# Kernel optimization log

Measured on AMD Instinct MI355X. Metric: run time of the kernel, lower is better.

## Reference

```python
import jax, jax.numpy as jnp
import numpy as np

B, C, H, W = 4, 384, 64, 64
NH = 8
HD = C // NH
SR = 2
SCALE = HD ** -0.5
Hs, Ws = H // SR, W // SR
NK = Hs * Ws


def setup_inputs() -> dict:
    key = jax.random.key(0)
    ks = jax.random.split(key, 8)
    s = 0.02
    return {
        "x": jax.random.normal(ks[0], (B, C, H, W), jnp.float32),
        "Wq": jax.random.normal(ks[1], (C, C), jnp.float32) * s,
        "Wk": jax.random.normal(ks[2], (C, C), jnp.float32) * s,
        "Wv": jax.random.normal(ks[3], (C, C), jnp.float32) * s,
        "Wsr": jax.random.normal(ks[4], (C, C, SR, SR), jnp.float32) * s,
        "bsr": jnp.zeros((C,), jnp.float32),
        "Wp": jax.random.normal(ks[5], (C, C), jnp.float32) * s,
        "bp": jnp.zeros((C,), jnp.float32),
        "rel_h": jax.random.normal(ks[6], (1, NH, HD, 1, Hs), jnp.float32),
        "rel_w": jax.random.normal(ks[7], (1, NH, HD, Ws, 1), jnp.float32),
    }


def _mhsa(x, Wq, Wk, Wv, Wsr, bsr, Wp, bp, rel_h, rel_w):
    Bq = x.shape[0]
    # 1x1 conv == channel matmul
    q = jnp.einsum('oc,bchw->bohw', Wq, x).reshape(Bq, NH, HD, H * W)
    # spatial reduction: Conv2d(kernel=SR, stride=SR); norm defaults to Identity
    xsr = jax.lax.conv_general_dilated(
        x, Wsr, window_strides=(SR, SR), padding='VALID',
        dimension_numbers=('NCHW', 'OIHW', 'NCHW')) + bsr[None, :, None, None]
    k = jnp.einsum('oc,bchw->bohw', Wk, xsr).reshape(Bq, NH, HD, NK)
    v = jnp.einsum('oc,bchw->bohw', Wv, xsr).reshape(Bq, NH, HD, NK)
    # relative positional bias fused into keys
    pos = (rel_h + rel_w).reshape(1, NH, HD, NK)
    k = (k + pos) * SCALE
    # attn[b,h,n,m] = q^T k, softmax over keys (dropout is identity at p=0)
    attn = jax.nn.softmax(jnp.einsum('bhdn,bhdm->bhnm', q, k), axis=-1)
    out = jnp.einsum('bhdm,bhnm->bhdn', v, attn).reshape(Bq, C, H, W)
    out = jnp.einsum('oc,bchw->bohw', Wp, out) + bp[None, :, None, None]
    return out


def reference(x, Wq, Wk, Wv, Wsr, bsr, Wp, bp, rel_h, rel_w):
    return _mhsa(x, Wq, Wk, Wv, Wsr, bsr, Wp, bp, rel_h, rel_w)
```

## Files before the change

### kernel.cpp

```cpp
#include <hip/hip_runtime.h>
#include <hip/hip_bf16.h>
#include <math.h>

typedef __attribute__((ext_vector_type(8))) short b16x8;
typedef __attribute__((ext_vector_type(4))) short b16x4;
typedef __attribute__((ext_vector_type(4))) float floatx4;
typedef __attribute__((ext_vector_type(16))) float f32x16;

constexpr int BATCH = 4, CCH = 384, NQ = 4096, NHD = 8, HDIM = 48, NK = 1024;
constexpr float SCALE_L2E = 0.14433756729740643f * 1.4426950408889634f;

__device__ inline unsigned short f2bf(float f) {
    unsigned u = __builtin_bit_cast(unsigned, f);
    u += 0x7fffu + ((u >> 16) & 1u);
    return (unsigned short)(u >> 16);
}

__device__ __forceinline__ void g2lds16(const void* g, void* l) {
    __builtin_amdgcn_global_load_lds(
        (const __attribute__((address_space(1))) unsigned int*)g,
        (__attribute__((address_space(3))) unsigned int*)l, 16, 0, 0);
}

__global__ void prep_kern(const float* __restrict__ Wq, const float* __restrict__ Wk,
                          const float* __restrict__ Wv, const float* __restrict__ Wsr,
                          const float* __restrict__ Wp, const float* __restrict__ x,
                          short* __restrict__ WqB, short* __restrict__ WkvB,
                          short* __restrict__ WsrB, short* __restrict__ WpB,
                          short* __restrict__ xT) {
    int job = blockIdx.y;
    if (job == 5) {
        for (int i = blockIdx.x * 256 + threadIdx.x; i < BATCH * 4096 * 48;
             i += 576 * 256) {
            int b = i / (4096 * 48);
            int rem = i - b * (4096 * 48);
            int c8 = rem / 4096, s = rem - c8 * 4096;
            b16x8 pk;
            #pragma unroll
            for (int e = 0; e < 8; e++)
                pk[e] = (short)f2bf(x[((size_t)b * CCH + c8 * 8 + e) * NQ + s]);
            *(b16x8*)(xT + ((size_t)b * NQ + s) * CCH + c8 * 8) = pk;
        }
        return;
    }
    if (job == 3) {
        for (int i = blockIdx.x * 256 + threadIdx.x; i < 589824; i += gridDim.x * 256) {
            int o = i / 1536, r = i - o * 1536;
            WsrB[o * 1536 + (r & 3) * 384 + (r >> 2)] = (short)f2bf(Wsr[i]);
        }
        return;
    }
    const float* src; short* dst;
    if (job == 0)      { src = Wq;  dst = WqB; }
    else if (job == 1) { src = Wk;  dst = WkvB; }
    else if (job == 2) { src = Wv;  dst = WkvB + 147456; }
    else               { src = Wp;  dst = WpB; }
    for (int i = blockIdx.x * 256 + threadIdx.x; i < 147456; i += gridDim.x * 256)
        dst[i] = (short)f2bf(src[i]);
}

__global__ __launch_bounds__(256, 2) void fused_gemm1(
    const short* __restrict__ WsrB, const short* __restrict__ WqB,
    const short* __restrict__ xT, const float* __restrict__ bsr,
    short* __restrict__ xsrT, short* __restrict__ qTb)
{
    __shared__ short At[128 * 64];
    __shared__ short Bt[128 * 64];
    const int b = blockIdx.z;
    const int id = blockIdx.x;
    const bool conv = id < 24;
    const int sx = conv ? (id & 7) : ((id - 24) & 31);
    const int oy = conv ? (id >> 3) : ((id - 24) >> 5);
    const int Ks = conv ? 1536 : 384;
    const int S  = conv ? NK : NQ;
    const short* A = conv ? WsrB : WqB;
    short* Yt = conv ? xsrT : qTb;
    const int o0 = oy * 128, s0 = sx * 128;
    const int t = threadIdx.x, wave = t >> 6, lane = t & 63, g = lane >> 4, li = lane & 15;
    const int wr = wave >> 1, wc = wave & 1;
    floatx4 acc[4][4] = {};
    const short* Bbase = xT + (size_t)b * NQ * CCH;

    for (int k0 = 0; k0 < Ks; k0 += 64) {
        __syncthreads();
        #pragma unroll
        for (int it = 0; it < 4; it++) {
            int task = it * 256 + t;
            int row = task >> 3, ch = task & 7;
            int cont = ch ^ (row & 7);
            g2lds16(A + (size_t)(o0 + row) * Ks + k0 + cont * 8, At + task * 8);
        }
        #pragma unroll
        for (int it = 0; it < 4; it++) {
            int task = it * 256 + t;
            int row = task >> 3, ch = task & 7;
            int cont = ch ^ (row & 7);
            if (conv) {
                int ssr = s0 + row;
                int hs = ssr >> 5, wsv = ssr & 31;
                int k = k0 + cont * 8;
                int p = k / 384, coff = k - p * 384;
                g2lds16(Bbase + (size_t)((2 * hs + (p >> 1)) * 64 + 2 * wsv + (p & 1)) * 384 + coff,
                        Bt + task * 8);
            } else {
                g2lds16(Bbase + (size_t)(s0 + row) * 384 + k0 + cont * 8, Bt + task * 8);
            }
        }
        __syncthreads();
        #pragma unroll
        for (int kk = 0; kk < 2; kk++) {
            b16x8 af[4], bf[4];
            #pragma unroll
            for (int mi = 0; mi < 4; mi++) {
                int r = wr * 64 + mi * 16 + li;
                af[mi] = *(const b16x8*)(At + r * 64 + (((kk * 4 + g) ^ (r & 7)) * 8));
            }
            #pragma unroll
            for (int nf = 0; nf < 4; nf++) {
                int r = wc * 64 + nf * 16 + li;
                bf[nf] = *(const b16x8*)(Bt + r * 64 + (((kk * 4 + g) ^ (r & 7)) * 8));
            }
            #pragma unroll
            for (int mi = 0; mi < 4; mi++)
                #pragma unroll
                for (int nf = 0; nf < 4; nf++)
                    acc[mi][nf] = __builtin_amdgcn_mfma_f32_16x16x32_bf16(af[mi], bf[nf], acc[mi][nf], 0, 0, 0);
        }
    }

    #pragma unroll
    for (int mi = 0; mi < 4; mi++) {
        #pragma unroll
        for (int nf = 0; nf < 4; nf++) {
            int o = o0 + wr * 64 + mi * 16 + g * 4;
            int s = s0 + wc * 64 + nf * 16 + li;
            b16x4 pk;
            #pragma unroll
            for (int j = 0; j < 4; j++) {
                float v = acc[mi][nf][j];
                if (conv) v += bsr[o + j];
                pk[j] = (short)f2bf(v);
            }
            *(b16x4*)(Yt + ((size_t)b * S + s) * CCH + o) = pk;
        }
    }
}

__global__ __launch_bounds__(256, 2) void kv_gemm(
    const short* __restrict__ WkvB, const short* __restrict__ xsrT,
    const float* __restrict__ relh, const float* __restrict__ relw,
    short* __restrict__ kTb, short* __restrict__ vCb)
{
    __shared__ short At[128 * 64];
    __shared__ short Bt[128 * 64];
    const int b = blockIdx.z, o0 = blockIdx.y * 128, s0 = blockIdx.x * 128;
    const int t = threadIdx.x, wave = t >> 6, lane = t & 63, g = lane >> 4, li = lane & 15;
    const int wr = wave >> 1, wc = wave & 1;
    floatx4 acc[4][4] = {};
    const short* Bbase = xsrT + (size_t)b * NK * CCH;

    for (int k0 = 0; k0 < 384; k0 += 64) {
        __syncthreads();
        #pragma unroll
        for (int it = 0; it < 4; it++) {
            int task = it * 256 + t;
            int row = task >> 3, ch = task & 7;
            int cont = ch ^ (row & 7);
            g2lds16(WkvB + (size_t)(o0 + row) * 384 + k0 + cont * 8, At + task * 8);
        }
        #pragma unroll
        for (int it = 0; it < 4; it++) {
            int task = it * 256 + t;
            int row = task >> 3, ch = task & 7;
            int cont = ch ^ (row & 7);
            g2lds16(Bbase + (size_t)(s0 + row) * 384 + k0 + cont * 8, Bt + task * 8);
        }
        __syncthreads();
        #pragma unroll
        for (int kk = 0; kk < 2; kk++) {
            b16x8 af[4], bf[4];
            #pragma unroll
            for (int mi = 0; mi < 4; mi++) {
                int r = wr * 64 + mi * 16 + li;
                af[mi] = *(const b16x8*)(At + r * 64 + (((kk * 4 + g) ^ (r & 7)) * 8));
            }
            #pragma unroll
            for (int nf = 0; nf < 4; nf++) {
                int r = wc * 64 + nf * 16 + li;
                bf[nf] = *(const b16x8*)(Bt + r * 64 + (((kk * 4 + g) ^ (r & 7)) * 8));
            }
            #pragma unroll
            for (int mi = 0; mi < 4; mi++)
                #pragma unroll
                for (int nf = 0; nf < 4; nf++)
                    acc[mi][nf] = __builtin_amdgcn_mfma_f32_16x16x32_bf16(af[mi], bf[nf], acc[mi][nf], 0, 0, 0);
        }
    }

    #pragma unroll
    for (int mi = 0; mi < 4; mi++) {
        #pragma unroll
        for (int nf = 0; nf < 4; nf++) {
            int o = o0 + wr * 64 + mi * 16 + g * 4;
            int s = s0 + wc * 64 + nf * 16 + li;
            if (o0 < 384) {
                int hs = s >> 5, wsv = s & 31;
                b16x4 pk;
                #pragma unroll
                for (int j = 0; j < 4; j++)
                    pk[j] = (short)f2bf((acc[mi][nf][j] + relh[(o + j) * 32 + wsv]
                                         + relw[(o + j) * 32 + hs]) * SCALE_L2E);
                *(b16x4*)(kTb + ((size_t)b * NK + s) * CCH + o) = pk;
            } else {
                #pragma unroll
                for (int j = 0; j < 4; j++)
                    vCb[((size_t)b * CCH + (o - 384 + j)) * NK + s] = (short)f2bf(acc[mi][nf][j]);
            }
        }
    }
}

__global__ __launch_bounds__(256, 2) void p_gemm(
    const short* __restrict__ A, const short* __restrict__ Bm,
    float* __restrict__ Yf, const float* __restrict__ bias)
{
    __shared__ short At[128 * 64];
    __shared__ short Bt[128 * 64];
    const int b = blockIdx.z, o0 = blockIdx.y * 128, s0 = blockIdx.x * 128;
    const int t = threadIdx.x, wave = t >> 6, lane = t & 63, g = lane >> 4, li = lane & 15;
    const int wr = wave >> 1, wc = wave & 1;
    floatx4 acc[4][4] = {};
    const short* Bbase = Bm + (size_t)b * NQ * CCH;

    for (int k0 = 0; k0 < 384; k0 += 64) {
        __syncthreads();
        #pragma unroll
        for (int it = 0; it < 4; it++) {
            int task = it * 256 + t;
            int row = task >> 3, ch = task & 7;
            int cont = ch ^ (row & 7);
            g2lds16(A + (size_t)(o0 + row) * 384 + k0 + cont * 8, At + task * 8);
        }
        #pragma unroll
        for (int it = 0; it < 4; it++) {
            int task = it * 256 + t;
            int row = task >> 3, ch = task & 7;
            int cont = ch ^ (row & 7);
            g2lds16(Bbase + (size_t)(s0 + row) * 384 + k0 + cont * 8, Bt + task * 8);
        }
        __syncthreads();
        #pragma unroll
        for (int kk = 0; kk < 2; kk++) {
            b16x8 af[4], bf[4];
            #pragma unroll
            for (int mi = 0; mi < 4; mi++) {
                int r = wr * 64 + mi * 16 + li;
                af[mi] = *(const b16x8*)(At + r * 64 + (((kk * 4 + g) ^ (r & 7)) * 8));
            }
            #pragma unroll
            for (int nf = 0; nf < 4; nf++) {
                int r = wc * 64 + nf * 16 + li;
                bf[nf] = *(const b16x8*)(Bt + r * 64 + (((kk * 4 + g) ^ (r & 7)) * 8));
            }
            #pragma unroll
            for (int mi = 0; mi < 4; mi++)
                #pragma unroll
                for (int nf = 0; nf < 4; nf++)
                    acc[mi][nf] = __builtin_amdgcn_mfma_f32_16x16x32_bf16(af[mi], bf[nf], acc[mi][nf], 0, 0, 0);
        }
    }

    #pragma unroll
    for (int mi = 0; mi < 4; mi++) {
        #pragma unroll
        for (int nf = 0; nf < 4; nf++) {
            int o = o0 + wr * 64 + mi * 16 + g * 4;
            int s = s0 + wc * 64 + nf * 16 + li;
            #pragma unroll
            for (int j = 0; j < 4; j++)
                Yf[((size_t)b * CCH + o + j) * (size_t)NQ + s] = acc[mi][nf][j] + bias[o + j];
        }
    }
}

__global__ __launch_bounds__(256, 3) void attn_kern(
    const short* __restrict__ qT, const short* __restrict__ kT,
    const short* __restrict__ vC, short* __restrict__ attT)
{
    __shared__ short Kl[3][6 * 64 * 8];
    __shared__ short Vl[3][8 * 64 * 8];
    const int wgid = blockIdx.x;
    const int nid = (wgid & 7) * 128 + (wgid >> 3);
    const int qt = nid & 31, hh = (nid >> 5) & 7, b = nid >> 8;
    const int t = threadIdx.x, wave = t >> 6, lane = t & 63;
    const int h = lane >> 5, c = lane & 31;
    const int n0 = qt * 128 + wave * 32;

    const short* qp = qT + (size_t)b * NQ * CCH + hh * HDIM;
    const short* kp = kT + (size_t)b * NK * CCH + hh * HDIM;
    const short* vp = vC + ((size_t)b * CCH + hh * HDIM) * NK;

    for (int i = t; i < 384; i += 256) {
        int bufi = i >> 7, rem = i & 127;
        int ch = rem >> 4, row = 48 + (rem & 15);
        b16x8 val = {};
        if (row == 48)
            #pragma unroll
            for (int e = 0; e < 8; e++) val[e] = (short)0x3F80;
        *(b16x8*)(&Vl[bufi][(ch * 64 + row) * 8]) = val;
    }
    asm volatile("s_waitcnt lgkmcnt(0)" ::: "memory");

    b16x8 qf[3];
    #pragma unroll
    for (int dc = 0; dc < 3; dc++)
        qf[dc] = *(const b16x8*)(qp + (size_t)(n0 + c) * CCH + dc * 16 + h * 8);
    asm volatile("s_waitcnt vmcnt(0)" ::: "memory");

    const int rowS = t & 63;
    const int chA = t >> 6;
    const int keyS = (rowS & 51) | ((rowS & 4) << 1) | ((rowS & 8) >> 1);
    const short* ksrcA = kp + (size_t)keyS * CCH + chA * 8;
    const bool  kvalB = (chA + 4) < 6;
    const bool  vval  = rowS < 48;
    const short* vsrcA = vp + (size_t)rowS * NK + chA * 8;
    const int taskA8 = t * 8, taskB8 = (t + 256) * 8;

    auto stage = [&](int m0, int bi) {
        size_t koff = (size_t)m0 * CCH;
        g2lds16(ksrcA + koff, &Kl[bi][taskA8]);
        if (kvalB) g2lds16(ksrcA + koff + 32, &Kl[bi][taskB8]);
        if (vval) {
            g2lds16(vsrcA + m0, &Vl[bi][taskA8]);
            g2lds16(vsrcA + m0 + 32, &Vl[bi][taskB8]);
        }
    };

    f32x16 O[2] = {};

    stage(0, 0);
    stage(64, 1);
    int cur = 0;
    for (int tt = 0; tt < 16; ++tt) {
        if (tt < 15) {
            if (wave < 2) asm volatile("s_waitcnt vmcnt(4)" ::: "memory");
            else          asm volatile("s_waitcnt vmcnt(3)" ::: "memory");
        } else {
            asm volatile("s_waitcnt vmcnt(0)" ::: "memory");
        }
        __builtin_amdgcn_s_barrier();
        const short* Kb = Kl[cur];
        const short* Vb = Vl[cur];
        #pragma unroll
        for (int kb = 0; kb < 2; kb++) {
            b16x8 kf[3];
            #pragma unroll
            for (int dc = 0; dc < 3; dc++)
                kf[dc] = *(const b16x8*)(Kb + (((dc * 2 + h) * 64) + kb * 32 + c) * 8);
            f32x16 s = {};
            __builtin_amdgcn_s_setprio(1);
            #pragma unroll
            for (int dc = 0; dc < 3; dc++)
                s = __builtin_amdgcn_mfma_f32_32x32x16_bf16(kf[dc], qf[dc], s, 0, 0, 0);
            __builtin_amdgcn_s_setprio(0);
            float p[16];
            #pragma unroll
            for (int r = 0; r < 16; r++)
                p[r] = __builtin_amdgcn_exp2f(s[r]);
            b16x8 pfrag[2];
            #pragma unroll
            for (int kk = 0; kk < 2; kk++) {
                union { unsigned u[4]; b16x8 v; } w;
                #pragma unroll
                for (int wd = 0; wd < 4; wd++)
                    asm("v_cvt_pk_bf16_f32 %0, %1, %2"
                        : "=v"(w.u[wd])
                        : "v"(p[kk * 8 + wd * 2]), "v"(p[kk * 8 + wd * 2 + 1]));
                pfrag[kk] = w.v;
            }
            __builtin_amdgcn_s_setprio(1);
            #pragma unroll
            for (int kk = 0; kk < 2; kk++)
                #pragma unroll
                for (int db = 0; db < 2; db++) {
                    b16x8 vf = *(const b16x8*)(Vb + (((kb * 4 + kk * 2 + h) * 64) + db * 32 + c) * 8);
                    O[db] = __builtin_amdgcn_mfma_f32_32x32x16_bf16(pfrag[kk], vf, O[db], 0, 0, 0);
                }
            __builtin_amdgcn_s_setprio(0);
        }
        if (tt < 14) {
            int nb = cur + 2; if (nb >= 3) nb -= 3;
            stage((tt + 2) * 64, nb);
        }
        cur = (cur == 2) ? 0 : cur + 1;
    }

    __syncthreads();
    short* Olw = ((short*)Vl) + wave * 2048;
    #pragma unroll
    for (int r = 0; r < 16; r++) {
        int qrow = (r & 3) + 8 * (r >> 2) + 4 * h;
        float lr = __shfl(O[1][r], (lane & 32) | 16);
        float iq = 1.0f / lr;
        #pragma unroll
        for (int db = 0; db < 2; db++) {
            int d = db * 32 + c;
            if (d < 48)
                Olw[qrow * 64 + (((d >> 3) ^ (qrow & 7)) * 8) + (d & 7)] =
                    (short)f2bf(O[db][r] * iq);
        }
    }
    #pragma unroll
    for (int it = 0; it < 4; it++) {
        int idx = it * 64 + lane;
        int row = idx >> 3, c8 = idx & 7;
        if (c8 < 6) {
            b16x8 val = *(const b16x8*)(Olw + row * 64 + ((c8 ^ (row & 7)) * 8));
            *(b16x8*)(attT + ((size_t)b * NQ + n0 + row) * CCH + hh * HDIM + c8 * 8) = val;
        }
    }
}

extern "C" void kernel_launch(void* const* d_in, const int* in_sizes, int n_in,
                              void* d_out, int out_size, void* d_ws, size_t ws_size,
                              hipStream_t stream) {
    const float* x    = (const float*)d_in[0];
    const float* Wq   = (const float*)d_in[1];
    const float* Wk   = (const float*)d_in[2];
    const float* Wv   = (const float*)d_in[3];
    const float* Wsr  = (const float*)d_in[4];
    const float* bsr  = (const float*)d_in[5];
    const float* Wp   = (const float*)d_in[6];
    const float* bp   = (const float*)d_in[7];
    const float* relh = (const float*)d_in[8];
    const float* relw = (const float*)d_in[9];
    float* out = (float*)d_out;

    short* ws = (short*)d_ws;
    size_t off = 0;
    auto alloc = [&](size_t n) { short* p = ws + off; off += n; return p; };
    short* WqB  = alloc(147456);
    short* WkvB = alloc(294912);
    short* WsrB = alloc(589824);
    short* WpB  = alloc(147456);
    short* xT   = alloc((size_t)BATCH * NQ * CCH);
    short* xsrT = alloc((size_t)BATCH * NK * CCH);
    short* qTb  = alloc((size_t)BATCH * NQ * CCH);
    short* kTb  = alloc((size_t)BATCH * NK * CCH);
    short* vCb  = alloc((size_t)BATCH * CCH * NK);
    short* attT = alloc((size_t)BATCH * NQ * CCH);

    prep_kern<<<dim3(576, 6), 256, 0, stream>>>(Wq, Wk, Wv, Wsr, Wp, x,
                                                WqB, WkvB, WsrB, WpB, xT);
    fused_gemm1<<<dim3(120, 1, BATCH), 256, 0, stream>>>(WsrB, WqB, xT, bsr, xsrT, qTb);
    kv_gemm<<<dim3(8, 6, BATCH), 256, 0, stream>>>(WkvB, xsrT, relh, relw, kTb, vCb);
    attn_kern<<<dim3(1024), 256, 0, stream>>>(qTb, kTb, vCb, attT);
    p_gemm<<<dim3(32, 3, BATCH), 256, 0, stream>>>(WpB, attT, out, bp);
}
```

Before: 119.4 us.

## Double attention workgroup size to share K/V tiles across eight waves

The attention kernel now runs 512 threads per workgroup, each covering 256 queries instead of 128, so each K/V tile staged in LDS serves twice as many query rows. The grid is halved. Loads are split by role: six waves each issue one K chunk and two waves issue four V chunks, with per-role vmcnt waits adjusted to match. This halves global K/V traffic per query, but wave specialization makes the load issue uneven and the larger blocks may change occupancy.

New measurement: 109.3 us, median of 2. -8.5%, faster.

```diff
diff --git a/kernel.cpp b/kernel.cpp
--- a/kernel.cpp
+++ b/kernel.cpp
@@ -283,31 +283,32 @@
     }
 }
 
-__global__ __launch_bounds__(256, 3) void attn_kern(
+__global__ __launch_bounds__(512, 4) void attn_kern(
     const short* __restrict__ qT, const short* __restrict__ kT,
     const short* __restrict__ vC, short* __restrict__ attT)
 {
-    __shared__ short Kl[3][6 * 64 * 8];
-    __shared__ short Vl[3][8 * 64 * 8];
+    __shared__ short SH[3 * 3072 + 3 * 4096];
+    short* const Klb = SH;
+    short* const Vlb = SH + 3 * 3072;
     const int wgid = blockIdx.x;
-    const int nid = (wgid & 7) * 128 + (wgid >> 3);
-    const int qt = nid & 31, hh = (nid >> 5) & 7, b = nid >> 8;
+    const int nid = (wgid & 7) * 64 + (wgid >> 3);
+    const int qt = nid & 15, hh = (nid >> 4) & 7, b = nid >> 7;
     const int t = threadIdx.x, wave = t >> 6, lane = t & 63;
     const int h = lane >> 5, c = lane & 31;
-    const int n0 = qt * 128 + wave * 32;
+    const int n0 = qt * 256 + wave * 32;
 
     const short* qp = qT + (size_t)b * NQ * CCH + hh * HDIM;
     const short* kp = kT + (size_t)b * NK * CCH + hh * HDIM;
     const short* vp = vC + ((size_t)b * CCH + hh * HDIM) * NK;
 
-    for (int i = t; i < 384; i += 256) {
-        int bufi = i >> 7, rem = i & 127;
+    if (t < 384) {
+        int bufi = t >> 7, rem = t & 127;
         int ch = rem >> 4, row = 48 + (rem & 15);
         b16x8 val = {};
         if (row == 48)
             #pragma unroll
             for (int e = 0; e < 8; e++) val[e] = (short)0x3F80;
-        *(b16x8*)(&Vl[bufi][(ch * 64 + row) * 8]) = val;
+        *(b16x8*)(Vlb + bufi * 4096 + (ch * 64 + row) * 8) = val;
     }
     asm volatile("s_waitcnt lgkmcnt(0)" ::: "memory");
 
@@ -317,22 +318,22 @@
         qf[dc] = *(const b16x8*)(qp + (size_t)(n0 + c) * CCH + dc * 16 + h * 8);
     asm volatile("s_waitcnt vmcnt(0)" ::: "memory");
 
-    const int rowS = t & 63;
-    const int chA = t >> 6;
-    const int keyS = (rowS & 51) | ((rowS & 4) << 1) | ((rowS & 8) >> 1);
-    const short* ksrcA = kp + (size_t)keyS * CCH + chA * 8;
-    const bool  kvalB = (chA + 4) < 6;
-    const bool  vval  = rowS < 48;
-    const short* vsrcA = vp + (size_t)rowS * NK + chA * 8;
-    const int taskA8 = t * 8, taskB8 = (t + 256) * 8;
+    const bool isK = t < 384;
+    const int krow = lane;
+    const int keyS = (krow & 51) | ((krow & 4) << 1) | ((krow & 8) >> 1);
+    const short* ksrc = kp + (size_t)keyS * CCH + wave * 8;
+    const int kdst8 = t * 8;
+    const int vch0 = (wave - 6) * 4;
+    const short* vrowsrc = vp + (size_t)lane * NK;
 
     auto stage = [&](int m0, int bi) {
-        size_t koff = (size_t)m0 * CCH;
-        g2lds16(ksrcA + koff, &Kl[bi][taskA8]);
-        if (kvalB) g2lds16(ksrcA + koff + 32, &Kl[bi][taskB8]);
-        if (vval) {
-            g2lds16(vsrcA + m0, &Vl[bi][taskA8]);
-            g2lds16(vsrcA + m0 + 32, &Vl[bi][taskB8]);
+        if (isK) {
+            g2lds16(ksrc + (size_t)m0 * CCH, Klb + bi * 3072 + kdst8);
+        } else if (lane < 48) {
+            short* vb = Vlb + bi * 4096;
+            #pragma unroll
+            for (int i = 0; i < 4; i++)
+                g2lds16(vrowsrc + (vch0 + i) * 8 + m0, vb + ((vch0 + i) * 64 + lane) * 8);
         }
     };
 
@@ -343,14 +344,14 @@
     int cur = 0;
     for (int tt = 0; tt < 16; ++tt) {
         if (tt < 15) {
-            if (wave < 2) asm volatile("s_waitcnt vmcnt(4)" ::: "memory");
-            else          asm volatile("s_waitcnt vmcnt(3)" ::: "memory");
+            if (isK) asm volatile("s_waitcnt vmcnt(1)" ::: "memory");
+            else     asm volatile("s_waitcnt vmcnt(4)" ::: "memory");
         } else {
             asm volatile("s_waitcnt vmcnt(0)" ::: "memory");
         }
         __builtin_amdgcn_s_barrier();
-        const short* Kb = Kl[cur];
-        const short* Vb = Vl[cur];
+        const short* Kb = Klb + cur * 3072;
+        const short* Vb = Vlb + cur * 4096;
         #pragma unroll
         for (int kb = 0; kb < 2; kb++) {
             b16x8 kf[3];
@@ -396,7 +397,7 @@
     }
 
     __syncthreads();
-    short* Olw = ((short*)Vl) + wave * 2048;
+    short* Olw = SH + wave * 2048;
     #pragma unroll
     for (int r = 0; r < 16; r++) {
         int qrow = (r & 3) + 8 * (r >> 2) + 4 * h;
@@ -454,6 +455,6 @@
                                                 WqB, WkvB, WsrB, WpB, xT);
     fused_gemm1<<<dim3(120, 1, BATCH), 256, 0, stream>>>(WsrB, WqB, xT, bsr, xsrT, qTb);
     kv_gemm<<<dim3(8, 6, BATCH), 256, 0, stream>>>(WkvB, xsrT, relh, relw, kTb, vCb);
-    attn_kern<<<dim3(1024), 256, 0, stream>>>(qTb, kTb, vCb, attT);
+    attn_kern<<<dim3(512), 512, 0, stream>>>(qTb, kTb, vCb, attT);
     p_gemm<<<dim3(32, 3, BATCH), 256, 0, stream>>>(WpB, attT, out, bp);
 }
```
